# Kernel tuning notes

Hardware: AMD Instinct MI355X
Metric: run time of the kernel (lower is better)

The kernel has to match this reference:

```python
import jax, jax.numpy as jnp
import numpy as np

MAX_LEN = 2048
D_MODEL = 1024
NUM_HEADS = 16
D_HEAD = D_MODEL // NUM_HEADS
BATCH = 2
SEQ = 2048


def setup_inputs() -> dict:
    key = jax.random.key(0)
    ks = jax.random.split(key, 8)
    scale = 1.0 / np.sqrt(D_MODEL)
    return {
        "x": jax.random.normal(ks[0], (BATCH, SEQ, D_MODEL), dtype=jnp.float32),
        "Wq": jax.random.normal(ks[1], (D_MODEL, D_MODEL), dtype=jnp.float32) * scale,
        "bq": jnp.zeros((D_MODEL,), dtype=jnp.float32),
        "Wk": jax.random.normal(ks[2], (D_MODEL, D_MODEL), dtype=jnp.float32) * scale,
        "bk": jnp.zeros((D_MODEL,), dtype=jnp.float32),
        "Wv": jax.random.normal(ks[3], (D_MODEL, D_MODEL), dtype=jnp.float32) * scale,
        "bv": jnp.zeros((D_MODEL,), dtype=jnp.float32),
        "Er": jax.random.normal(ks[4], (MAX_LEN, D_HEAD), dtype=jnp.float32),
    }


def _skew(QEr):
    # QEr: [B, H, S, S] -> Transformer-XL skew -> Srel: [B, H, S, S]
    B, H, S, _ = QEr.shape
    padded = jnp.pad(QEr, ((0, 0), (0, 0), (0, 0), (1, 0)))  # [B,H,S,S+1]
    reshaped = padded.reshape(B, H, S + 1, S)
    return reshaped[:, :, 1:, :]


def reference(x, Wq, bq, Wk, bk, Wv, bv, Er):
    B, S, D = x.shape
    H, dh = NUM_HEADS, D // NUM_HEADS
    q = (x @ Wq + bq).reshape(B, S, H, dh).transpose(0, 2, 1, 3)  # [B,H,S,dh]
    k = (x @ Wk + bk).reshape(B, S, H, dh).transpose(0, 2, 1, 3)
    v = (x @ Wv + bv).reshape(B, S, H, dh).transpose(0, 2, 1, 3)
    Er_s = Er[MAX_LEN - S:, :]                                    # [S, dh]
    QEr = jnp.einsum("bhsd,ld->bhsl", q, Er_s)                    # [B,H,S,S]
    Srel = _skew(QEr)
    QKt = jnp.einsum("bhsd,bhtd->bhst", q, k)
    attn = (QKt + Srel) / jnp.sqrt(jnp.asarray(dh, x.dtype))
    causal = jnp.tril(jnp.ones((S, S), dtype=bool))
    attn = jnp.where(causal[None, None], attn, -jnp.inf)
    attn = jax.nn.softmax(attn, axis=-1)
    out = jnp.einsum("bhst,bhtd->bhsd", attn, v)                  # [B,H,S,dh]
    return out.transpose(0, 2, 1, 3).reshape(B, S, D)             # dropout in eval = identity
```

## Files before the change

kernel.cpp:

```cpp
#include <hip/hip_runtime.h>
#include <hip/hip_bf16.h>

#define SLEN   2048
#define DMODEL 1024
#define NHEADS 16
#define DHEAD  64
#define NBATCH 2
#define EPAD_ROWS 2432

typedef __bf16 bf16x8 __attribute__((ext_vector_type(8)));
typedef float  f32x4  __attribute__((ext_vector_type(4)));

__device__ __forceinline__ unsigned short f2bf(float f) {
    unsigned int u = __builtin_bit_cast(unsigned int, f);
    return (unsigned short)((u + 0x7fffu + ((u >> 16) & 1u)) >> 16);
}

__device__ __forceinline__ unsigned short f2bf_hw(float f) {
    return __builtin_bit_cast(unsigned short, (__bf16)f);
}

__device__ __forceinline__ bf16x8 ld8(const unsigned short* p) {
    union { uint4 u; bf16x8 b; } t;
    t.u = *(const uint4*)p;
    return t.b;
}

__device__ __forceinline__ void glds16(const unsigned short* g, unsigned short* l) {
    __builtin_amdgcn_global_load_lds(
        (const __attribute__((address_space(1))) unsigned int*)g,
        (__attribute__((address_space(3))) unsigned int*)l, 16, 0, 0);
}

__global__ __launch_bounds__(256) void prep_kernel(
    const float* __restrict__ x, const float* __restrict__ Er,
    const float* __restrict__ Wq, const float* __restrict__ Wk,
    const float* __restrict__ Wv,
    unsigned short* __restrict__ xb, unsigned short* __restrict__ Ep,
    unsigned short* __restrict__ Wt) {
    const int bi = blockIdx.x, tid = threadIdx.x;
    if (bi < 4096) {
        int i = (bi * 256 + tid) * 4;
        float4 v = *(const float4*)(x + i);
        ushort4 o;
        o.x = f2bf(v.x); o.y = f2bf(v.y); o.z = f2bf(v.z); o.w = f2bf(v.w);
        *(ushort4*)(xb + i) = o;
    } else if (bi < 4704) {
        int i = (bi - 4096) * 256 + tid;
        int row = i >> 6;
        unsigned short v = 0;
        if (row < SLEN) v = f2bf(Er[i]);
        Ep[i] = v;
    } else {
        __shared__ float tile[32][33];
        const int b3 = bi - 4704;
        const int z = b3 >> 10, rem = b3 & 1023;
        const int n0 = (rem & 31) * 32, k0 = (rem >> 5) * 32;
        const float* W = (z == 0) ? Wq : (z == 1 ? Wk : Wv);
        unsigned short* out = Wt + (size_t)z * DMODEL * DMODEL;
        const int tx = tid & 31, ty = tid >> 5;
        for (int r = 0; r < 32; r += 8)
            tile[ty + r][tx] = W[(size_t)(k0 + ty + r) * DMODEL + n0 + tx];
        __syncthreads();
        for (int r = 0; r < 32; r += 8)
            out[(size_t)(n0 + ty + r) * DMODEL + k0 + tx] = f2bf(tile[tx][ty + r]);
    }
}

__global__ __launch_bounds__(256) void qkv_gemm(
    const unsigned short* __restrict__ xb, const unsigned short* __restrict__ Wt,
    const float* __restrict__ bq, const float* __restrict__ bk, const float* __restrict__ bv,
    unsigned short* __restrict__ Qs, unsigned short* __restrict__ Ks,
    unsigned short* __restrict__ Vts) {
    const int z = blockIdx.z;
    const float* bias = (z == 0) ? bq : (z == 1 ? bk : bv);
    const unsigned short* Wz = Wt + (size_t)z * DMODEL * DMODEL;
    const int m0 = blockIdx.y * 128, n0 = blockIdx.x * 128;

    __shared__ __align__(16) unsigned short As[2][128][64];
    __shared__ __align__(16) unsigned short Bs[2][128][64];

    const int tid = threadIdx.x;
    const int wave = tid >> 6, lane = tid & 63, l16 = lane & 15, quad = lane >> 4;
    const int wm = (wave >> 1) * 64, wn = (wave & 1) * 64;

    const int lr8 = lane >> 3;
    const int sc  = ((lane & 7) ^ lr8) * 8;

    f32x4 acc[4][4];
#pragma unroll
    for (int mi = 0; mi < 4; mi++)
#pragma unroll
        for (int ni = 0; ni < 4; ni++) acc[mi][ni] = (f32x4){0.f, 0.f, 0.f, 0.f};

#pragma unroll
    for (int c = 0; c < 4; c++) {
        const int seg = wave * 4 + c;
        const int r8  = seg * 8 + lr8;
        glds16(&xb[(size_t)(m0 + r8) * DMODEL + sc], &As[0][seg * 8][0]);
        glds16(&Wz[(size_t)(n0 + r8) * DMODEL + sc], &Bs[0][seg * 8][0]);
    }
    __syncthreads();

    for (int j = 0; j < 16; ++j) {
        const int cur = j & 1;
        if (j < 15) {
            const int k1 = (j + 1) * 64, nb = cur ^ 1;
#pragma unroll
            for (int c = 0; c < 4; c++) {
                const int seg = wave * 4 + c;
                const int r8  = seg * 8 + lr8;
                glds16(&xb[(size_t)(m0 + r8) * DMODEL + k1 + sc], &As[nb][seg * 8][0]);
                glds16(&Wz[(size_t)(n0 + r8) * DMODEL + k1 + sc], &Bs[nb][seg * 8][0]);
            }
        }
        const unsigned short (*Aarr)[64] = (z == 2) ? Bs[cur] : As[cur];
        const unsigned short (*Barr)[64] = (z == 2) ? As[cur] : Bs[cur];
#pragma unroll
        for (int ks = 0; ks < 2; ks++) {
            const int pc = ((ks * 4 + quad) ^ (l16 & 7)) * 8;
            bf16x8 a[4], b[4];
#pragma unroll
            for (int mi = 0; mi < 4; mi++) a[mi] = ld8(&Aarr[wm + mi * 16 + l16][pc]);
#pragma unroll
            for (int ni = 0; ni < 4; ni++) b[ni] = ld8(&Barr[wn + ni * 16 + l16][pc]);
#pragma unroll
            for (int mi = 0; mi < 4; mi++)
#pragma unroll
                for (int ni = 0; ni < 4; ni++)
                    acc[mi][ni] = __builtin_amdgcn_mfma_f32_16x16x32_bf16(a[mi], b[ni], acc[mi][ni], 0, 0, 0);
        }
        __syncthreads();
    }

    if (z == 2) {
#pragma unroll
        for (int mi = 0; mi < 4; mi++)
#pragma unroll
            for (int r = 0; r < 4; r++) {
                const int n = n0 + wm + mi * 16 + quad * 4 + r;
                const float bb = bias[n];
                const int h = n >> 6, d = n & 63;
#pragma unroll
                for (int ni = 0; ni < 4; ni++) {
                    const int m = m0 + wn + ni * 16 + l16;
                    const int bi = m >> 11, s = m & 2047;
                    Vts[((size_t)((bi * NHEADS + h) * 64 + d)) * SLEN + s] = f2bf(acc[mi][ni][r] + bb);
                }
            }
    } else {
#pragma unroll
        for (int ni = 0; ni < 4; ni++) {
            const int n = n0 + wn + ni * 16 + l16;
            const float bb = bias[n];
            const int h = n >> 6, d = n & 63;
#pragma unroll
            for (int mi = 0; mi < 4; mi++)
#pragma unroll
                for (int r = 0; r < 4; r++) {
                    const int m = m0 + wm + mi * 16 + quad * 4 + r;
                    const int bi = m >> 11, s = m & 2047;
                    float v = acc[mi][ni][r] + bb;
                    if (z == 0)
                        Qs[((size_t)(bi * NHEADS + h) * SLEN + s) * 64 + d] = f2bf(v * 0.125f);
                    else
                        Ks[((size_t)(bi * NHEADS + h) * SLEN + s) * 64 + d] = f2bf(v);
                }
        }
    }
}

__global__ __launch_bounds__(256, 2) void attn_kernel(
    const unsigned short* __restrict__ Q,
    const unsigned short* __restrict__ K,
    const unsigned short* __restrict__ Vt,
    const unsigned short* __restrict__ Ep,
    float* __restrict__ out) {
    const int tid = threadIdx.x;
    const int wave = tid >> 6, lane = tid & 63, l16 = lane & 15, quad = lane >> 4;
    const int lr8 = lane >> 3;
    const int swz = ((lane & 7) ^ lr8) * 8;

    const int bh = blockIdx.x & 31;
    const int pg = blockIdx.x >> 5;

    __shared__ __align__(16) unsigned short Ksh[2][64 * 64];
    __shared__ __align__(16) unsigned short Vsh[2][64 * 64];
    __shared__ __align__(16) unsigned short Esh[256 * 64];
    __shared__ __align__(16) unsigned short Pg[4][16][88];

    const unsigned short* Qb = Q + (size_t)bh * SLEN * 64;
    const unsigned short* Kb = K + (size_t)bh * SLEN * 64;
    const unsigned short* Vb = Vt + (size_t)bh * 64 * SLEN;
    const int ob = bh >> 4, oh = bh & 15;

    const int pc0 = (quad ^ (l16 & 7)) * 8;
    const int pc1 = ((4 + quad) ^ (l16 & 7)) * 8;
    int perm[4];
    bool hi[4];
#pragma unroll
    for (int r = 0; r < 4; r++) {
        const int row16 = quad * 4 + r;
        perm[r] = (quad << 4) | ((l16 + 15 - row16) & 15);
        hi[r] = (l16 + row16 >= 15);
    }

    int s0 = pg * 64;
    int ntp = pg + 1;

#pragma unroll 1
    for (int pass = 0; pass < 2; ++pass) {
        const int sw = s0 + 16 * wave;
        const bf16x8 aq0 = ld8(Qb + (size_t)(sw + l16) * 64 + quad * 8);
        const bf16x8 aq1 = ld8(Qb + (size_t)(sw + l16) * 64 + 32 + quad * 8);

        f32x4 accO[4];
        float sacc[4];
#pragma unroll
        for (int nt = 0; nt < 4; nt++) accO[nt] = (f32x4){0.f, 0.f, 0.f, 0.f};
#pragma unroll
        for (int r = 0; r < 4; r++) sacc[r] = 0.f;

        const int p0row = SLEN - 64 - s0;

#pragma unroll
        for (int c = 0; c < 2; c++) {
            const int seg = wave * 2 + c;
            glds16(&Kb[(size_t)(seg * 8 + lr8) * 64 + swz], &Ksh[0][seg * 8 * 64]);
            glds16(&Vb[(size_t)(seg * 8 + lr8) * SLEN + swz], &Vsh[0][seg * 8 * 64]);
        }
#pragma unroll
        for (int u = 0; u < 6; u++) {
            const int idx = wave * 6 + u;
            const int grow = p0row + idx * 8;
            glds16(&Ep[(size_t)(grow + lr8) * 64 + swz], &Esh[(grow & 255) * 64]);
        }
        __syncthreads();

        for (int j = 0; j < ntp; ++j) {
            const int t0 = j * 64;
            const int cur = j & 1;

            if (j + 1 < ntp) {
                const int t1 = t0 + 64, nb = cur ^ 1;
#pragma unroll
                for (int c = 0; c < 2; c++) {
                    const int seg = wave * 2 + c;
                    glds16(&Kb[(size_t)(t1 + seg * 8 + lr8) * 64 + swz], &Ksh[nb][seg * 8 * 64]);
                    glds16(&Vb[(size_t)(seg * 8 + lr8) * SLEN + t1 + swz], &Vsh[nb][seg * 8 * 64]);
                }
                const int er = p0row + t0 + 128;
#pragma unroll
                for (int c = 0; c < 2; c++) {
                    const int seg = wave * 2 + c;
                    glds16(&Ep[(size_t)(er + seg * 8 + lr8) * 64 + swz],
                           &Esh[((er + seg * 8) & 255) * 64]);
                }
            }

            f32x4 accS[4];
#pragma unroll
            for (int nt = 0; nt < 4; nt++) accS[nt] = (f32x4){0.f, 0.f, 0.f, 0.f};
#pragma unroll
            for (int nt = 0; nt < 4; nt++) {
                bf16x8 bk0 = ld8(&Ksh[cur][(nt * 16 + l16) * 64 + pc0]);
                bf16x8 bk1 = ld8(&Ksh[cur][(nt * 16 + l16) * 64 + pc1]);
                accS[nt] = __builtin_amdgcn_mfma_f32_16x16x32_bf16(aq0, bk0, accS[nt], 0, 0, 0);
                accS[nt] = __builtin_amdgcn_mfma_f32_16x16x32_bf16(aq1, bk1, accS[nt], 0, 0, 0);
            }

            const int rm0 = (SLEN - 16 - sw + t0) & 255;
            f32x4 accE[5];
#pragma unroll
            for (int nt = 0; nt < 5; nt++) accE[nt] = (f32x4){0.f, 0.f, 0.f, 0.f};
#pragma unroll
            for (int nt = 0; nt < 5; nt++) {
                const int rowm = (rm0 + nt * 16 + l16) & 255;
                bf16x8 be0 = ld8(&Esh[rowm * 64 + pc0]);
                bf16x8 be1 = ld8(&Esh[rowm * 64 + pc1]);
                accE[nt] = __builtin_amdgcn_mfma_f32_16x16x32_bf16(aq0, be0, accE[nt], 0, 0, 0);
                accE[nt] = __builtin_amdgcn_mfma_f32_16x16x32_bf16(aq1, be1, accE[nt], 0, 0, 0);
            }

            auto scoreblk = [&](bool masked) {
#pragma unroll
                for (int nt = 0; nt < 4; nt++) {
#pragma unroll
                    for (int r = 0; r < 4; r++) {
                        float send = hi[r] ? accE[nt][r] : accE[nt + 1][r];
                        float rel = __shfl(send, perm[r]);
                        float pexp = __expf(accS[nt][r] + rel - 16.0f);
                        if (masked)
                            pexp = (t0 + nt * 16 + l16 <= sw + quad * 4 + r) ? pexp : 0.0f;
                        sacc[r] += pexp;
                        Pg[wave][quad * 4 + r][nt * 16 + l16] = f2bf_hw(pexp);
                    }
                }
            };
            if (t0 + 63 <= sw) scoreblk(false);
            else               scoreblk(true);

            bf16x8 a0 = ld8(&Pg[wave][l16][quad * 8]);
            bf16x8 a1 = ld8(&Pg[wave][l16][32 + quad * 8]);
#pragma unroll
            for (int nt = 0; nt < 4; nt++) {
                bf16x8 bv0 = ld8(&Vsh[cur][(nt * 16 + l16) * 64 + pc0]);
                bf16x8 bv1 = ld8(&Vsh[cur][(nt * 16 + l16) * 64 + pc1]);
                accO[nt] = __builtin_amdgcn_mfma_f32_16x16x32_bf16(a0, bv0, accO[nt], 0, 0, 0);
                accO[nt] = __builtin_amdgcn_mfma_f32_16x16x32_bf16(a1, bv1, accO[nt], 0, 0, 0);
            }

            __syncthreads();
        }

#pragma unroll
        for (int r = 0; r < 4; r++) {
            float s4 = sacc[r];
#pragma unroll
            for (int off = 1; off < 16; off <<= 1) s4 += __shfl_xor(s4, off);
            const float inv = 1.f / s4;
            const int s = sw + quad * 4 + r;
#pragma unroll
            for (int nt = 0; nt < 4; nt++)
                out[((size_t)(ob * SLEN + s)) * DMODEL + oh * 64 + nt * 16 + l16] =
                    accO[nt][r] * inv;
        }

        s0 = (31 - pg) * 64;
        ntp = 32 - pg;
    }
}

extern "C" void kernel_launch(void* const* d_in, const int* in_sizes, int n_in,
                              void* d_out, int out_size, void* d_ws, size_t ws_size,
                              hipStream_t stream) {
    const float* x  = (const float*)d_in[0];
    const float* Wq = (const float*)d_in[1];
    const float* bq = (const float*)d_in[2];
    const float* Wk = (const float*)d_in[3];
    const float* bk = (const float*)d_in[4];
    const float* Wv = (const float*)d_in[5];
    const float* bv = (const float*)d_in[6];
    const float* Er = (const float*)d_in[7];
    float* out = (float*)d_out;

    char* p = (char*)d_ws;
    unsigned short* xb  = (unsigned short*)p; p += (size_t)4096 * 1024 * 2;
    unsigned short* Wt  = (unsigned short*)p; p += (size_t)3 * 1024 * 1024 * 2;
    unsigned short* Qs  = (unsigned short*)p; p += (size_t)32 * 2048 * 64 * 2;
    unsigned short* Ks  = (unsigned short*)p; p += (size_t)32 * 2048 * 64 * 2;
    unsigned short* Vts = (unsigned short*)p; p += (size_t)32 * 2048 * 64 * 2;
    unsigned short* Ep  = (unsigned short*)p; p += (size_t)EPAD_ROWS * 64 * 2;

    hipLaunchKernelGGL(prep_kernel, dim3(7776), dim3(256), 0, stream,
                       x, Er, Wq, Wk, Wv, xb, Ep, Wt);
    hipLaunchKernelGGL(qkv_gemm, dim3(8, 32, 3), dim3(256), 0, stream,
                       xb, Wt, bq, bk, bv, Qs, Ks, Vts);
    hipLaunchKernelGGL(attn_kernel, dim3(512), dim3(256), 0, stream, Qs, Ks, Vts, Ep, out);
}
```

Before: 187.9 us.

## Load Er fragments directly from global and fold softmax scale into exp2

Drops the 32KB shared-memory ring buffer for the relative-position embedding Er. Each wave now loads its Er fragments directly from global memory into registers every tile. The softmax scale log2(e)/8 is folded into Q, and the constant offset is folded into the accumulator init, so the exponent becomes a bare exp2. Cutting shared memory may raise occupancy and removes LDS traffic, but adds per-wave global loads that are only partly reused, through cache.

```diff
diff --git a/kernel.cpp b/kernel.cpp
--- a/kernel.cpp
+++ b/kernel.cpp
@@ -7,6 +7,9 @@
 #define DHEAD  64
 #define NBATCH 2
 #define EPAD_ROWS 2432
+
+#define QSCALE 0.18033688011112042f
+#define EXPB   23.083120654223414f
 
 typedef __bf16 bf16x8 __attribute__((ext_vector_type(8)));
 typedef float  f32x4  __attribute__((ext_vector_type(4)));
@@ -162,7 +165,7 @@
                     const int bi = m >> 11, s = m & 2047;
                     float v = acc[mi][ni][r] + bb;
                     if (z == 0)
-                        Qs[((size_t)(bi * NHEADS + h) * SLEN + s) * 64 + d] = f2bf(v * 0.125f);
+                        Qs[((size_t)(bi * NHEADS + h) * SLEN + s) * 64 + d] = f2bf(v * QSCALE);
                     else
                         Ks[((size_t)(bi * NHEADS + h) * SLEN + s) * 64 + d] = f2bf(v);
                 }
@@ -186,7 +189,6 @@
 
     __shared__ __align__(16) unsigned short Ksh[2][64 * 64];
     __shared__ __align__(16) unsigned short Vsh[2][64 * 64];
-    __shared__ __align__(16) unsigned short Esh[256 * 64];
     __shared__ __align__(16) unsigned short Pg[4][16][88];
 
     const unsigned short* Qb = Q + (size_t)bh * SLEN * 64;
@@ -221,25 +223,26 @@
 #pragma unroll
         for (int r = 0; r < 4; r++) sacc[r] = 0.f;
 
-        const int p0row = SLEN - 64 - s0;
-
 #pragma unroll
         for (int c = 0; c < 2; c++) {
             const int seg = wave * 2 + c;
             glds16(&Kb[(size_t)(seg * 8 + lr8) * 64 + swz], &Ksh[0][seg * 8 * 64]);
             glds16(&Vb[(size_t)(seg * 8 + lr8) * SLEN + swz], &Vsh[0][seg * 8 * 64]);
         }
-#pragma unroll
-        for (int u = 0; u < 6; u++) {
-            const int idx = wave * 6 + u;
-            const int grow = p0row + idx * 8;
-            glds16(&Ep[(size_t)(grow + lr8) * 64 + swz], &Esh[(grow & 255) * 64]);
-        }
         __syncthreads();
 
         for (int j = 0; j < ntp; ++j) {
             const int t0 = j * 64;
             const int cur = j & 1;
+
+            const int er0 = SLEN - 16 - sw + t0;
+            bf16x8 be[5][2];
+#pragma unroll
+            for (int nt = 0; nt < 5; nt++) {
+                const unsigned short* ep = Ep + (size_t)(er0 + nt * 16 + l16) * 64 + quad * 8;
+                be[nt][0] = ld8(ep);
+                be[nt][1] = ld8(ep + 32);
+            }
 
             if (j + 1 < ntp) {
                 const int t1 = t0 + 64, nb = cur ^ 1;
@@ -249,18 +252,12 @@
                     glds16(&Kb[(size_t)(t1 + seg * 8 + lr8) * 64 + swz], &Ksh[nb][seg * 8 * 64]);
                     glds16(&Vb[(size_t)(seg * 8 + lr8) * SLEN + t1 + swz], &Vsh[nb][seg * 8 * 64]);
                 }
-                const int er = p0row + t0 + 128;
-#pragma unroll
-                for (int c = 0; c < 2; c++) {
-                    const int seg = wave * 2 + c;
-                    glds16(&Ep[(size_t)(er + seg * 8 + lr8) * 64 + swz],
-                           &Esh[((er + seg * 8) & 255) * 64]);
-                }
             }
 
             f32x4 accS[4];
 #pragma unroll
-            for (int nt = 0; nt < 4; nt++) accS[nt] = (f32x4){0.f, 0.f, 0.f, 0.f};
+            for (int nt = 0; nt < 4; nt++)
+                accS[nt] = (f32x4){-EXPB, -EXPB, -EXPB, -EXPB};
 #pragma unroll
             for (int nt = 0; nt < 4; nt++) {
                 bf16x8 bk0 = ld8(&Ksh[cur][(nt * 16 + l16) * 64 + pc0]);
@@ -269,17 +266,13 @@
                 accS[nt] = __builtin_amdgcn_mfma_f32_16x16x32_bf16(aq1, bk1, accS[nt], 0, 0, 0);
             }
 
-            const int rm0 = (SLEN - 16 - sw + t0) & 255;
             f32x4 accE[5];
 #pragma unroll
             for (int nt = 0; nt < 5; nt++) accE[nt] = (f32x4){0.f, 0.f, 0.f, 0.f};
 #pragma unroll
             for (int nt = 0; nt < 5; nt++) {
-                const int rowm = (rm0 + nt * 16 + l16) & 255;
-                bf16x8 be0 = ld8(&Esh[rowm * 64 + pc0]);
-                bf16x8 be1 = ld8(&Esh[rowm * 64 + pc1]);
-                accE[nt] = __builtin_amdgcn_mfma_f32_16x16x32_bf16(aq0, be0, accE[nt], 0, 0, 0);
-                accE[nt] = __builtin_amdgcn_mfma_f32_16x16x32_bf16(aq1, be1, accE[nt], 0, 0, 0);
+                accE[nt] = __builtin_amdgcn_mfma_f32_16x16x32_bf16(aq0, be[nt][0], accE[nt], 0, 0, 0);
+                accE[nt] = __builtin_amdgcn_mfma_f32_16x16x32_bf16(aq1, be[nt][1], accE[nt], 0, 0, 0);
             }
 
             auto scoreblk = [&](bool masked) {
@@ -289,7 +282,7 @@
                     for (int r = 0; r < 4; r++) {
                         float send = hi[r] ? accE[nt][r] : accE[nt + 1][r];
                         float rel = __shfl(send, perm[r]);
-                        float pexp = __expf(accS[nt][r] + rel - 16.0f);
+                        float pexp = __builtin_exp2f(accS[nt][r] + rel);
                         if (masked)
                             pexp = (t0 + nt * 16 + l16 <= sw + quad * 4 + r) ? pexp : 0.0f;
                         sacc[r] += pexp;
```

Result: slower. 216.4 us (+15.2%).

## Fold log2e into Q scale and drop double buffering in QKV GEMM

Applied to the files above, without the earlier changes.

The 1/sqrt(dh) query scale now also carries log2(e), so the softmax can call exp2 directly. The constant offset is folded into the MFMA accumulator initial value, which removes a subtract and a multiply per score element. Separately, the QKV GEMM drops its double-buffered LDS for a single buffer with a sync before compute, and raises the occupancy hint to 3 blocks per CU. This trades load/compute overlap for higher occupancy. The bf16 rounding of the rescaled Q changes numerics slightly.

```diff
diff --git a/kernel.cpp b/kernel.cpp
--- a/kernel.cpp
+++ b/kernel.cpp
@@ -7,6 +7,9 @@
 #define DHEAD  64
 #define NBATCH 2
 #define EPAD_ROWS 2432
+
+#define QSCALE 0.18033688011112042f
+#define EXPB   23.083120654223414f
 
 typedef __bf16 bf16x8 __attribute__((ext_vector_type(8)));
 typedef float  f32x4  __attribute__((ext_vector_type(4)));
@@ -67,7 +70,7 @@
     }
 }
 
-__global__ __launch_bounds__(256) void qkv_gemm(
+__global__ __launch_bounds__(256, 3) void qkv_gemm(
     const unsigned short* __restrict__ xb, const unsigned short* __restrict__ Wt,
     const float* __restrict__ bq, const float* __restrict__ bk, const float* __restrict__ bv,
     unsigned short* __restrict__ Qs, unsigned short* __restrict__ Ks,
@@ -77,8 +80,8 @@
     const unsigned short* Wz = Wt + (size_t)z * DMODEL * DMODEL;
     const int m0 = blockIdx.y * 128, n0 = blockIdx.x * 128;
 
-    __shared__ __align__(16) unsigned short As[2][128][64];
-    __shared__ __align__(16) unsigned short Bs[2][128][64];
+    __shared__ __align__(16) unsigned short As[128][64];
+    __shared__ __align__(16) unsigned short Bs[128][64];
 
     const int tid = threadIdx.x;
     const int wave = tid >> 6, lane = tid & 63, l16 = lane & 15, quad = lane >> 4;
@@ -93,29 +96,20 @@
 #pragma unroll
         for (int ni = 0; ni < 4; ni++) acc[mi][ni] = (f32x4){0.f, 0.f, 0.f, 0.f};
 
-#pragma unroll
-    for (int c = 0; c < 4; c++) {
-        const int seg = wave * 4 + c;
-        const int r8  = seg * 8 + lr8;
-        glds16(&xb[(size_t)(m0 + r8) * DMODEL + sc], &As[0][seg * 8][0]);
-        glds16(&Wz[(size_t)(n0 + r8) * DMODEL + sc], &Bs[0][seg * 8][0]);
-    }
-    __syncthreads();
-
     for (int j = 0; j < 16; ++j) {
-        const int cur = j & 1;
-        if (j < 15) {
-            const int k1 = (j + 1) * 64, nb = cur ^ 1;
-#pragma unroll
-            for (int c = 0; c < 4; c++) {
-                const int seg = wave * 4 + c;
-                const int r8  = seg * 8 + lr8;
-                glds16(&xb[(size_t)(m0 + r8) * DMODEL + k1 + sc], &As[nb][seg * 8][0]);
-                glds16(&Wz[(size_t)(n0 + r8) * DMODEL + k1 + sc], &Bs[nb][seg * 8][0]);
-            }
-        }
-        const unsigned short (*Aarr)[64] = (z == 2) ? Bs[cur] : As[cur];
-        const unsigned short (*Barr)[64] = (z == 2) ? As[cur] : Bs[cur];
+        if (j) __syncthreads();
+        const int k0 = j * 64;
+#pragma unroll
+        for (int c = 0; c < 4; c++) {
+            const int seg = wave * 4 + c;
+            const int r8  = seg * 8 + lr8;
+            glds16(&xb[(size_t)(m0 + r8) * DMODEL + k0 + sc], &As[seg * 8][0]);
+            glds16(&Wz[(size_t)(n0 + r8) * DMODEL + k0 + sc], &Bs[seg * 8][0]);
+        }
+        __syncthreads();
+
+        const unsigned short (*Aarr)[64] = (z == 2) ? Bs : As;
+        const unsigned short (*Barr)[64] = (z == 2) ? As : Bs;
 #pragma unroll
         for (int ks = 0; ks < 2; ks++) {
             const int pc = ((ks * 4 + quad) ^ (l16 & 7)) * 8;
@@ -130,7 +124,6 @@
                 for (int ni = 0; ni < 4; ni++)
                     acc[mi][ni] = __builtin_amdgcn_mfma_f32_16x16x32_bf16(a[mi], b[ni], acc[mi][ni], 0, 0, 0);
         }
-        __syncthreads();
     }
 
     if (z == 2) {
@@ -162,7 +155,7 @@
                     const int bi = m >> 11, s = m & 2047;
                     float v = acc[mi][ni][r] + bb;
                     if (z == 0)
-                        Qs[((size_t)(bi * NHEADS + h) * SLEN + s) * 64 + d] = f2bf(v * 0.125f);
+                        Qs[((size_t)(bi * NHEADS + h) * SLEN + s) * 64 + d] = f2bf(v * QSCALE);
                     else
                         Ks[((size_t)(bi * NHEADS + h) * SLEN + s) * 64 + d] = f2bf(v);
                 }
@@ -260,7 +253,8 @@
 
             f32x4 accS[4];
 #pragma unroll
-            for (int nt = 0; nt < 4; nt++) accS[nt] = (f32x4){0.f, 0.f, 0.f, 0.f};
+            for (int nt = 0; nt < 4; nt++)
+                accS[nt] = (f32x4){-EXPB, -EXPB, -EXPB, -EXPB};
 #pragma unroll
             for (int nt = 0; nt < 4; nt++) {
                 bf16x8 bk0 = ld8(&Ksh[cur][(nt * 16 + l16) * 64 + pc0]);
@@ -289,7 +283,7 @@
                     for (int r = 0; r < 4; r++) {
                         float send = hi[r] ? accE[nt][r] : accE[nt + 1][r];
                         float rel = __shfl(send, perm[r]);
-                        float pexp = __expf(accS[nt][r] + rel - 16.0f);
+                        float pexp = __builtin_exp2f(accS[nt][r] + rel);
                         if (masked)
                             pexp = (t0 + nt * 16 + l16 <= sw + quad * 4 + r) ? pexp : 0.0f;
                         sacc[r] += pexp;
```

After: 180.2 us. -4.1%, faster.
